# Optimization experiments

Hardware: AMD Instinct MI355X
Metric: run time of the kernel (lower is better)

## Reference

```python
import jax, jax.numpy as jnp
import numpy as np

BATCH = 4096        # config['batch_size']
N_PARTS = 4         # config['n_parts']
TEMP = 0.1          # config['temp_fac']
D = 256             # embedding dim
BS = 3 * BATCH      # bs = 3 * batch_size
EPS = 1e-6          # CosineSimilarity eps


def setup_inputs() -> dict:
    key = jax.random.key(0)
    reg_pred = jax.random.normal(key, (BS, D), dtype=jnp.float32)
    return {"reg_pred": reg_pred}


def reference(reg_pred):
    B, bs, t = BATCH, BS, TEMP
    # cosine similarity: x/max(||x||, eps)
    nrm = jnp.linalg.norm(reg_pred, axis=1, keepdims=True)
    xn = reg_pred / jnp.maximum(nrm, EPS)
    E = jnp.exp((xn @ xn.T) / t)                      # exp(cos_sim/temp), [bs, bs]

    # negative-index mask: for anchor row a (pos_index p = a % B),
    # excluded indices are range(rem, bs, 4) with rem = p % n_parts
    k = jnp.arange(bs)
    rem = (k % B) % N_PARTS                           # rem per anchor row, [bs]
    excluded = (k[None, :] >= rem[:, None]) & (((k[None, :] - rem[:, None]) % 4) == 0)
    den = jnp.sum(jnp.where(excluded, 0.0, E), axis=1)  # [bs], sum exp(den sims)

    p = jnp.arange(B)
    i1, i2, i3 = p, B + p, 2 * B + p

    def pair_loss(a, b, n):
        # symmetrical NT-Xent-style term; n = exp(num_sim / t)
        return -jnp.log(n / (n + den[a])) - jnp.log(n / (n + den[b]))

    n12 = E[i1, i2]
    n13 = E[i1, i3]
    n23 = E[i2, i3]
    total = jnp.sum(pair_loss(i1, i2, n12)
                    + pair_loss(i1, i3, n13)
                    + pair_loss(i2, i3, n23))
    return total / (2 * B)
```

## Files before the change

### kernel.cpp

```cpp
#include <hip/hip_runtime.h>
#include <hip/hip_bf16.h>
#include <cstdint>
#include <cstddef>

#define BS_TOT 12288
#define DIM    256
#define BATCH_ 4096
#define NTILE  96

typedef float f32x16 __attribute__((ext_vector_type(16)));

__global__ __launch_bounds__(256) void normalize_kernel(const float* __restrict__ x,
                                                        uint8_t* __restrict__ xn,
                                                        float* __restrict__ invn,
                                                        float* __restrict__ den,
                                                        float* __restrict__ out,
                                                        int osz) {
  if (blockIdx.x == 0 && (int)threadIdx.x < osz) out[threadIdx.x] = 0.0f;
  const int wave = threadIdx.x >> 6;
  const int lane = threadIdx.x & 63;
  const int row  = blockIdx.x * 4 + wave;
  const float4 v = ((const float4*)(x + (size_t)row * DIM))[lane];
  float ss = v.x*v.x + v.y*v.y + v.z*v.z + v.w*v.w;
  #pragma unroll
  for (int off = 1; off < 64; off <<= 1) ss += __shfl_xor(ss, off, 64);
  const float s = 1.0f / fmaxf(sqrtf(ss), 1e-6f);
  if (lane == 0) { invn[row] = s; den[row] = 0.0f; }
  unsigned int w = __builtin_amdgcn_cvt_pk_fp8_f32(v.x * s, v.y * s, 0u, false);
  w = __builtin_amdgcn_cvt_pk_fp8_f32(v.z * s, v.w * s, w, true);
  ((unsigned int*)(xn + (size_t)row * DIM))[lane] = w;
}

__global__ __launch_bounds__(256, 2) void gemm_den_kernel(const uint8_t* __restrict__ xn,
                                                          float* __restrict__ den) {
  __shared__ unsigned long long As[128 * 32];
  __shared__ unsigned long long Bs[128 * 32];

  const int tid = threadIdx.x;
  const int tJ  = blockIdx.x;
  const int tI  = blockIdx.y;

  const int wave = tid >> 6, lane = tid & 63;
  const int wr   = wave >> 1, wc = wave & 1;
  const int l31  = lane & 31, half = lane >> 5;

  const uint8_t* Ab = xn + (size_t)tI * 128 * DIM;
  const uint8_t* Bb = xn + (size_t)tJ * 128 * DIM;

  ulonglong2 chA[8], chB[8];
  #pragma unroll
  for (int c = 0; c < 8; c++) {
    const int q = c * 256 + tid;
    const size_t off = (size_t)(q >> 4) * DIM + (size_t)(q & 15) * 16;
    chA[c] = *(const ulonglong2*)(Ab + off);
    chB[c] = *(const ulonglong2*)(Bb + off);
  }
  #pragma unroll
  for (int c = 0; c < 8; c++) {
    const int q = c * 256 + tid;
    const int row = q >> 4, k16 = q & 15;
    const int s0 = row * 32 + ((2 * k16)     ^ (row & 31));
    const int s1 = row * 32 + ((2 * k16 + 1) ^ (row & 31));
    As[s0] = chA[c].x; As[s1] = chA[c].y;
    Bs[s0] = chB[c].x; Bs[s1] = chB[c].y;
  }
  __syncthreads();

  f32x16 acc[2][2] = {};
  #pragma unroll
  for (int ks = 0; ks < 16; ks++) {
    long af[2], bf[2];
    #pragma unroll
    for (int mi = 0; mi < 2; mi++) {
      const int row = wr * 64 + mi * 32 + l31;
      af[mi] = (long)As[row * 32 + ((2 * ks + half) ^ (row & 31))];
    }
    #pragma unroll
    for (int ni = 0; ni < 2; ni++) {
      const int row = wc * 64 + ni * 32 + l31;
      bf[ni] = (long)Bs[row * 32 + ((2 * ks + half) ^ (row & 31))];
    }
    #pragma unroll
    for (int mi = 0; mi < 2; mi++)
      #pragma unroll
      for (int ni = 0; ni < 2; ni++)
        acc[mi][ni] = __builtin_amdgcn_mfma_f32_32x32x16_fp8_fp8(af[mi], bf[ni], acc[mi][ni], 0, 0, 0);
  }

  const int colBase = tJ * 128 + wc * 64;
  #pragma unroll
  for (int ni = 0; ni < 2; ni++) {
    float cs = 0.0f;
    #pragma unroll
    for (int mi = 0; mi < 2; mi++)
      #pragma unroll
      for (int r = 0; r < 16; r++)
        if (((l31 ^ r) & 3) != 0)
          cs += __expf(acc[mi][ni][r] * 10.0f);
    cs += __shfl_xor(cs, 32, 64);
    if (half == 0) atomicAdd(&den[colBase + ni * 32 + l31], cs);
  }
}

__global__ __launch_bounds__(256) void loss_kernel(const float* __restrict__ x,
                                                   const float* __restrict__ invn,
                                                   const float* __restrict__ den,
                                                   float* __restrict__ out) {
  __shared__ float part[4];
  const int wave = threadIdx.x >> 6, lane = threadIdx.x & 63;
  const int p = blockIdx.x * 4 + wave;
  const float4 a = ((const float4*)(x + (size_t)p * DIM))[lane];
  const float4 b = ((const float4*)(x + (size_t)(BATCH_ + p) * DIM))[lane];
  const float4 c = ((const float4*)(x + (size_t)(2*BATCH_ + p) * DIM))[lane];
  float d12 = a.x*b.x + a.y*b.y + a.z*b.z + a.w*b.w;
  float d13 = a.x*c.x + a.y*c.y + a.z*c.z + a.w*c.w;
  float d23 = b.x*c.x + b.y*c.y + b.z*c.z + b.w*c.w;
  #pragma unroll
  for (int off = 1; off < 64; off <<= 1) {
    d12 += __shfl_xor(d12, off, 64);
    d13 += __shfl_xor(d13, off, 64);
    d23 += __shfl_xor(d23, off, 64);
  }
  if (lane == 0) {
    const float s1 = invn[p], s2 = invn[BATCH_ + p], s3 = invn[2*BATCH_ + p];
    const float z12 = d12 * s1 * s2 * 10.0f;
    const float z13 = d13 * s1 * s3 * 10.0f;
    const float z23 = d23 * s2 * s3 * 10.0f;
    const float n12 = __expf(z12), n13 = __expf(z13), n23 = __expf(z23);
    const float e1 = den[p], e2 = den[BATCH_ + p], e3 = den[2*BATCH_ + p];
    part[wave] = logf(n12 + e1) + logf(n12 + e2) - 2.0f * z12
               + logf(n13 + e1) + logf(n13 + e3) - 2.0f * z13
               + logf(n23 + e2) + logf(n23 + e3) - 2.0f * z23;
  }
  __syncthreads();
  if (threadIdx.x == 0) {
    atomicAdd(out, (part[0] + part[1] + part[2] + part[3]) * (1.0f / (2.0f * BATCH_)));
  }
}

extern "C" void kernel_launch(void* const* d_in, const int* in_sizes, int n_in,
                              void* d_out, int out_size, void* d_ws, size_t ws_size,
                              hipStream_t stream) {
  const float* x = (const float*)d_in[0];
  float* out = (float*)d_out;

  char* ws = (char*)d_ws;
  uint8_t* xn   = (uint8_t*)ws;
  float*   invn = (float*)(ws + (size_t)BS_TOT * DIM);
  float*   den  = (float*)(ws + (size_t)BS_TOT * DIM + BS_TOT * 4);

  normalize_kernel<<<BS_TOT / 4, 256, 0, stream>>>(x, xn, invn, den, out, out_size);
  gemm_den_kernel<<<dim3(NTILE, NTILE), 256, 0, stream>>>(xn, den);
  loss_kernel<<<BATCH_ / 4, 256, 0, stream>>>(x, invn, den, out);
}
```

Measured before the change: 140.7 us.

## Exploit Gram matrix symmetry by computing only upper-triangular tiles

Launches only the upper-triangular tile pairs of the symmetric similarity matrix. Each off-diagonal tile contributes both column sums and row sums to the denominators, using wave shuffles and extra atomics for the row sums. The 1/temp scale is folded into the fp8 quantization by multiplying by sqrt(10), which removes the per-element multiply before exp. The loss uses fast __logf. This roughly halves the MFMA and exp work, at the cost of more shuffles and atomics, and of fp8 rounding applied to larger values.

```diff
diff --git a/kernel.cpp b/kernel.cpp
--- a/kernel.cpp
+++ b/kernel.cpp
@@ -7,6 +7,7 @@
 #define DIM    256
 #define BATCH_ 4096
 #define NTILE  96
+#define NPAIR  4656
 
 typedef float f32x16 __attribute__((ext_vector_type(16)));
 
@@ -26,8 +27,9 @@
   for (int off = 1; off < 64; off <<= 1) ss += __shfl_xor(ss, off, 64);
   const float s = 1.0f / fmaxf(sqrtf(ss), 1e-6f);
   if (lane == 0) { invn[row] = s; den[row] = 0.0f; }
-  unsigned int w = __builtin_amdgcn_cvt_pk_fp8_f32(v.x * s, v.y * s, 0u, false);
-  w = __builtin_amdgcn_cvt_pk_fp8_f32(v.z * s, v.w * s, w, true);
+  const float sc = s * 3.16227766016838f;
+  unsigned int w = __builtin_amdgcn_cvt_pk_fp8_f32(v.x * sc, v.y * sc, 0u, false);
+  w = __builtin_amdgcn_cvt_pk_fp8_f32(v.z * sc, v.w * sc, w, true);
   ((unsigned int*)(xn + (size_t)row * DIM))[lane] = w;
 }
 
@@ -37,8 +39,13 @@
   __shared__ unsigned long long Bs[128 * 32];
 
   const int tid = threadIdx.x;
-  const int tJ  = blockIdx.x;
-  const int tI  = blockIdx.y;
+
+  const int t = blockIdx.x;
+  int j = (int)((sqrtf(8.0f * (float)t + 1.0f) - 1.0f) * 0.5f);
+  while ((j + 1) * (j + 2) / 2 <= t) j++;
+  while (j * (j + 1) / 2 > t) j--;
+  const int tI = t - j * (j + 1) / 2;
+  const int tJ = j;
 
   const int wave = tid >> 6, lane = tid & 63;
   const int wr   = wave >> 1, wc = wave & 1;
@@ -87,17 +94,35 @@
         acc[mi][ni] = __builtin_amdgcn_mfma_f32_32x32x16_fp8_fp8(af[mi], bf[ni], acc[mi][ni], 0, 0, 0);
   }
 
+  const int rowBase = tI * 128 + wr * 64;
   const int colBase = tJ * 128 + wc * 64;
+  const bool offd = (tI != tJ);
+  float colsum[2] = {0.f, 0.f};
+
+  #pragma unroll
+  for (int mi = 0; mi < 2; mi++) {
+    #pragma unroll
+    for (int r = 0; r < 16; r++) {
+      const bool inc = ((l31 ^ r) & 3) != 0;
+      const float e0 = inc ? __expf(acc[mi][0][r]) : 0.0f;
+      const float e1 = inc ? __expf(acc[mi][1][r]) : 0.0f;
+      colsum[0] += e0;
+      colsum[1] += e1;
+      if (offd) {
+        float rv = e0 + e1;
+        rv += __shfl_xor(rv, 1, 64);
+        rv += __shfl_xor(rv, 2, 64);
+        rv += __shfl_xor(rv, 4, 64);
+        rv += __shfl_xor(rv, 8, 64);
+        rv += __shfl_xor(rv, 16, 64);
+        if (l31 == 0)
+          atomicAdd(&den[rowBase + mi*32 + (r & 3) + 8*(r >> 2) + 4*half], rv);
+      }
+    }
+  }
   #pragma unroll
   for (int ni = 0; ni < 2; ni++) {
-    float cs = 0.0f;
-    #pragma unroll
-    for (int mi = 0; mi < 2; mi++)
-      #pragma unroll
-      for (int r = 0; r < 16; r++)
-        if (((l31 ^ r) & 3) != 0)
-          cs += __expf(acc[mi][ni][r] * 10.0f);
-    cs += __shfl_xor(cs, 32, 64);
+    float cs = colsum[ni] + __shfl_xor(colsum[ni], 32, 64);
     if (half == 0) atomicAdd(&den[colBase + ni * 32 + l31], cs);
   }
 }
@@ -128,9 +153,9 @@
     const float z23 = d23 * s2 * s3 * 10.0f;
     const float n12 = __expf(z12), n13 = __expf(z13), n23 = __expf(z23);
     const float e1 = den[p], e2 = den[BATCH_ + p], e3 = den[2*BATCH_ + p];
-    part[wave] = logf(n12 + e1) + logf(n12 + e2) - 2.0f * z12
-               + logf(n13 + e1) + logf(n13 + e3) - 2.0f * z13
-               + logf(n23 + e2) + logf(n23 + e3) - 2.0f * z23;
+    part[wave] = __logf(n12 + e1) + __logf(n12 + e2) - 2.0f * z12
+               + __logf(n13 + e1) + __logf(n13 + e3) - 2.0f * z13
+               + __logf(n23 + e2) + __logf(n23 + e3) - 2.0f * z23;
   }
   __syncthreads();
   if (threadIdx.x == 0) {
@@ -150,6 +175,6 @@
   float*   den  = (float*)(ws + (size_t)BS_TOT * DIM + BS_TOT * 4);
 
   normalize_kernel<<<BS_TOT / 4, 256, 0, stream>>>(x, xn, invn, den, out, out_size);
-  gemm_den_kernel<<<dim3(NTILE, NTILE), 256, 0, stream>>>(xn, den);
+  gemm_den_kernel<<<NPAIR, 256, 0, stream>>>(xn, den);
   loss_kernel<<<BATCH_ / 4, 256, 0, stream>>>(x, invn, den, out);
 }
```

Measured after the change: 186.1 us. 1.32x slower.

## Use gfx950 32x32x64 scaled FP8 MFMA and fold temperature into normalization

Applied to the files above, without the earlier changes.

The GEMM moves from the 32x32x16 FP8 MFMA to the MI355X 32x32x64 scaled f8f6f4 MFMA, so each wave issues a quarter as many matrix instructions and loads 32-byte fragments from a re-swizzled byte-addressed LDS tile. The 1/temperature factor is folded into normalization by scaling each vector by sqrt(10), which removes the multiply before exp in the epilogue. It also switches logf to __logf in the loss kernel. Scaling inputs by sqrt(10) changes the FP8 quantization range and may affect accuracy, and the new LDS swizzle has to avoid bank conflicts on the wider reads.

```diff
diff --git a/kernel.cpp b/kernel.cpp
--- a/kernel.cpp
+++ b/kernel.cpp
@@ -9,6 +9,7 @@
 #define NTILE  96
 
 typedef float f32x16 __attribute__((ext_vector_type(16)));
+typedef int   i32x8  __attribute__((ext_vector_type(8)));
 
 __global__ __launch_bounds__(256) void normalize_kernel(const float* __restrict__ x,
                                                         uint8_t* __restrict__ xn,
@@ -26,15 +27,25 @@
   for (int off = 1; off < 64; off <<= 1) ss += __shfl_xor(ss, off, 64);
   const float s = 1.0f / fmaxf(sqrtf(ss), 1e-6f);
   if (lane == 0) { invn[row] = s; den[row] = 0.0f; }
-  unsigned int w = __builtin_amdgcn_cvt_pk_fp8_f32(v.x * s, v.y * s, 0u, false);
-  w = __builtin_amdgcn_cvt_pk_fp8_f32(v.z * s, v.w * s, w, true);
+  const float sc = s * 3.16227766016838f;
+  unsigned int w = __builtin_amdgcn_cvt_pk_fp8_f32(v.x * sc, v.y * sc, 0u, false);
+  w = __builtin_amdgcn_cvt_pk_fp8_f32(v.z * sc, v.w * sc, w, true);
   ((unsigned int*)(xn + (size_t)row * DIM))[lane] = w;
+}
+
+__device__ __forceinline__ i32x8 ld_frag32(const uint8_t* p) {
+  const int4 lo = *(const int4*)p;
+  const int4 hi = *(const int4*)(p + 16);
+  i32x8 r;
+  r[0] = lo.x; r[1] = lo.y; r[2] = lo.z; r[3] = lo.w;
+  r[4] = hi.x; r[5] = hi.y; r[6] = hi.z; r[7] = hi.w;
+  return r;
 }
 
 __global__ __launch_bounds__(256, 2) void gemm_den_kernel(const uint8_t* __restrict__ xn,
                                                           float* __restrict__ den) {
-  __shared__ unsigned long long As[128 * 32];
-  __shared__ unsigned long long Bs[128 * 32];
+  __shared__ __align__(16) uint8_t As[128 * 256];
+  __shared__ __align__(16) uint8_t Bs[128 * 256];
 
   const int tid = threadIdx.x;
   const int tJ  = blockIdx.x;
@@ -47,44 +58,46 @@
   const uint8_t* Ab = xn + (size_t)tI * 128 * DIM;
   const uint8_t* Bb = xn + (size_t)tJ * 128 * DIM;
 
-  ulonglong2 chA[8], chB[8];
+  int4 chA[8], chB[8];
   #pragma unroll
   for (int c = 0; c < 8; c++) {
     const int q = c * 256 + tid;
     const size_t off = (size_t)(q >> 4) * DIM + (size_t)(q & 15) * 16;
-    chA[c] = *(const ulonglong2*)(Ab + off);
-    chB[c] = *(const ulonglong2*)(Bb + off);
+    chA[c] = *(const int4*)(Ab + off);
+    chB[c] = *(const int4*)(Bb + off);
   }
   #pragma unroll
   for (int c = 0; c < 8; c++) {
-    const int q = c * 256 + tid;
+    const int q   = c * 256 + tid;
     const int row = q >> 4, k16 = q & 15;
-    const int s0 = row * 32 + ((2 * k16)     ^ (row & 31));
-    const int s1 = row * 32 + ((2 * k16 + 1) ^ (row & 31));
-    As[s0] = chA[c].x; As[s1] = chA[c].y;
-    Bs[s0] = chB[c].x; Bs[s1] = chB[c].y;
+    const int wa  = row * 256 + (((k16 >> 1) ^ (row & 7)) * 32) + (k16 & 1) * 16;
+    *(int4*)(As + wa) = chA[c];
+    *(int4*)(Bs + wa) = chB[c];
   }
   __syncthreads();
 
+  const int e7 = l31 & 7;
+  const int rowA0 = (wr * 64 + l31) * 256;
+  const int rowB0 = (wc * 64 + l31) * 256;
+
   f32x16 acc[2][2] = {};
   #pragma unroll
-  for (int ks = 0; ks < 16; ks++) {
-    long af[2], bf[2];
-    #pragma unroll
-    for (int mi = 0; mi < 2; mi++) {
-      const int row = wr * 64 + mi * 32 + l31;
-      af[mi] = (long)As[row * 32 + ((2 * ks + half) ^ (row & 31))];
-    }
-    #pragma unroll
-    for (int ni = 0; ni < 2; ni++) {
-      const int row = wc * 64 + ni * 32 + l31;
-      bf[ni] = (long)Bs[row * 32 + ((2 * ks + half) ^ (row & 31))];
-    }
+  for (int ks = 0; ks < 4; ks++) {
+    const int u = ((2 * ks + half) ^ e7) * 32;
+    i32x8 af[2], bf[2];
+    af[0] = ld_frag32(As + rowA0 + u);
+    af[1] = ld_frag32(As + rowA0 + 32 * 256 + u);
+    bf[0] = ld_frag32(Bs + rowB0 + u);
+    bf[1] = ld_frag32(Bs + rowB0 + 32 * 256 + u);
     #pragma unroll
     for (int mi = 0; mi < 2; mi++)
       #pragma unroll
       for (int ni = 0; ni < 2; ni++)
-        acc[mi][ni] = __builtin_amdgcn_mfma_f32_32x32x16_fp8_fp8(af[mi], bf[ni], acc[mi][ni], 0, 0, 0);
+        acc[mi][ni] = __builtin_amdgcn_mfma_scale_f32_32x32x64_f8f6f4(
+            af[mi], bf[ni], acc[mi][ni],
+            0, 0,
+            0, 0x7F7F7F7F,
+            0, 0x7F7F7F7F);
   }
 
   const int colBase = tJ * 128 + wc * 64;
@@ -96,7 +109,7 @@
       #pragma unroll
       for (int r = 0; r < 16; r++)
         if (((l31 ^ r) & 3) != 0)
-          cs += __expf(acc[mi][ni][r] * 10.0f);
+          cs += __expf(acc[mi][ni][r]);
     cs += __shfl_xor(cs, 32, 64);
     if (half == 0) atomicAdd(&den[colBase + ni * 32 + l31], cs);
   }
@@ -128,9 +141,9 @@
     const float z23 = d23 * s2 * s3 * 10.0f;
     const float n12 = __expf(z12), n13 = __expf(z13), n23 = __expf(z23);
     const float e1 = den[p], e2 = den[BATCH_ + p], e3 = den[2*BATCH_ + p];
-    part[wave] = logf(n12 + e1) + logf(n12 + e2) - 2.0f * z12
-               + logf(n13 + e1) + logf(n13 + e3) - 2.0f * z13
-               + logf(n23 + e2) + logf(n23 + e3) - 2.0f * z23;
+    part[wave] = __logf(n12 + e1) + __logf(n12 + e2) - 2.0f * z12
+               + __logf(n13 + e1) + __logf(n13 + e3) - 2.0f * z13
+               + __logf(n23 + e2) + __logf(n23 + e3) - 2.0f * z23;
   }
   __syncthreads();
   if (threadIdx.x == 0) {
```

Result: faster. 131.5 us (-6.6%).
